# Optimization experiments

Hardware: AMD Instinct MI355X
Metric: run time of the kernel (lower is better)

Reference implementation:

```python
import jax, jax.numpy as jnp
import numpy as np

EPS = 1e-6
NEG = -100000.0


def _ln(x):
    # LayerNorm, elementwise_affine=False, eps=1e-6
    mu = jnp.mean(x, axis=-1, keepdims=True)
    var = jnp.mean((x - mu) ** 2, axis=-1, keepdims=True)
    return (x - mu) * jax.lax.rsqrt(var + EPS)


def _split_heads(x, h):
    b, s, d = x.shape
    return x.reshape(b, s, h, d // h).transpose(0, 2, 1, 3)  # [B,H,S,Dh]


def _merge_heads(x):
    b, h, s, dh = x.shape
    return x.transpose(0, 2, 1, 3).reshape(b, s, h * dh)


def _conv_pool(x, w):
    # grouped Conv2d(num_heads -> num_heads, kernel=(4,1), stride=(4,1), groups=num_heads, bias=False)
    # x: [B,H,S,Dh] as NCHW, w: [H,1,4,1] as OIHW
    return jax.lax.conv_general_dilated(
        x, w, window_strides=(4, 1), padding='VALID',
        dimension_numbers=('NCHW', 'OIHW', 'NCHW'),
        feature_group_count=x.shape[1])


def setup_inputs() -> dict:
    key = jax.random.key(0)
    ks = jax.random.split(key, 14)
    B, S, M, D, QKV, MLP, H = 4, 4096, 256, 768, 768, 3072, 12
    std = 0.02
    f = lambda k, shp: jax.random.normal(k, shp, jnp.float32) * std
    return {
        'x': jax.random.normal(ks[0], (B, S, D), jnp.float32),
        'memory': jax.random.normal(ks[1], (B, M, D), jnp.float32),
        'mask': jax.random.randint(ks[2], (B, S), 0, 2).astype(jnp.int32),
        'Wq': f(ks[3], (QKV, D)), 'Wk': f(ks[4], (QKV, D)),
        'Wv': f(ks[5], (QKV, D)), 'Wo': f(ks[6], (D, QKV)),
        'conv_w': f(ks[7], (H, 1, 4, 1)),
        'Uq': f(ks[8], (QKV, D)), 'Uk': f(ks[9], (QKV, D)),
        'Uv': f(ks[10], (QKV, D)), 'Uo': f(ks[11], (D, QKV)),
        'W1': f(ks[12], (MLP, D)), 'W2': f(ks[13], (D, MLP)),
    }


def reference(x, memory, mask, Wq, Wk, Wv, Wo, conv_w, Uq, Uk, Uv, Uo, W1, W2):
    H = conv_w.shape[0]
    maskf = mask.astype(x.dtype)                       # [B,S]

    # ---- pack: ConvAttention(memory as q, x as k/v); conv downsamples k/v ->
    #      shape_change=True so the k_mask is skipped (as in the torch code).
    q = _split_heads(memory @ Wq.T, H)                 # [B,H,M,Dh], unit temperature (log_temp=0)
    k = _split_heads(x @ Wk.T, H)                      # [B,H,S,Dh]
    v = _split_heads(x @ Wv.T, H)
    k = _conv_pool(k, conv_w)                          # [B,H,S//4,Dh]
    v = _conv_pool(v, conv_w)
    logits = jnp.einsum('bhqd,bhkd->bhqk', q, k)
    att = jax.nn.softmax(logits, axis=-1)
    packed = _merge_heads(att @ v) @ Wo.T              # [B,M,D]

    # ---- unpack: TAttention(x as q, packed as k/v) with q_mask injection
    head_dim = Uq.shape[0] // H
    uq = _split_heads(x @ Uq.T, H) * (1.0 / jnp.sqrt(jnp.asarray(head_dim, x.dtype)))
    uk = _split_heads(packed @ Uk.T, H)                # [B,H,M,Dh]
    uv = _split_heads(packed @ Uv.T, H)
    ulogits = jnp.einsum('bhqd,bhkd->bhqk', uq, uk)    # [B,H,S,M]
    ulogits = ulogits + NEG * (1.0 - maskf[:, None, :, None])
    uatt = jax.nn.softmax(ulogits, axis=-1)
    unpacked = _merge_heads(uatt @ uv) @ Uo.T          # [B,S,D]

    unpacked = unpacked * maskf[..., None]
    q_out = _ln(x + unpacked)
    m_out = _ln(memory + packed)

    # FFN: Linear -> GELU(exact) -> Linear (dropout=0)
    h = jax.nn.gelu(jnp.einsum('bsd,md->bsm', q_out, W1), approximate=False)
    y = jnp.einsum('bsm,dm->bsd', h, W2)
    y = y * maskf[..., None]
    q_out = _ln(q_out + y)
    return (q_out, m_out)
```

## Files before the change

### kernel.cpp

```cpp
#include <hip/hip_runtime.h>
#include <hip/hip_bf16.h>
#include <math.h>


typedef unsigned short u16;
typedef __attribute__((ext_vector_type(8))) short bf8v;
typedef __attribute__((ext_vector_type(4))) float f4v;
typedef __attribute__((ext_vector_type(4))) unsigned short us4v;

#define AS1 __attribute__((address_space(1)))
#define AS3 __attribute__((address_space(3)))

__device__ __forceinline__ void gld_lds16(const void* g, void* l) {
  __builtin_amdgcn_global_load_lds((const AS1 unsigned int*)g,
                                   (AS3 unsigned int*)l, 16, 0, 0);
}

__device__ __forceinline__ u16 bf16_rne(float x) {
  unsigned u = __float_as_uint(x);
  return (u16)((u + 0x7fffu + ((u >> 16) & 1u)) >> 16);
}
__device__ __forceinline__ float bf16_to_f(u16 h) {
  return __uint_as_float(((unsigned)h) << 16);
}

__global__ __launch_bounds__(256) void tobf16_kernel(
    const float* __restrict__ in, u16* __restrict__ o, int n4, float scale) {
  int i = blockIdx.x * 256 + threadIdx.x;
  if (i >= n4) return;
  float4 v = ((const float4*)in)[i];
  us4v h;
  h[0] = bf16_rne(v.x * scale); h[1] = bf16_rne(v.y * scale);
  h[2] = bf16_rne(v.z * scale); h[3] = bf16_rne(v.w * scale);
  ((us4v*)o)[i] = h;
}

template <int BN, int GELU, int OMODE>
__global__ __launch_bounds__(256) void bgemm_kernel(
    const u16* __restrict__ A, const u16* __restrict__ B,
    float* __restrict__ Cf, u16* __restrict__ Cb, int M, int N, int K,
    int lda, int ldb, int ldc, long long aSB, long long aSH, long long bSB,
    long long bSH, long long cSB, long long cSH, int HB, float scale) {
  constexpr int NJ = BN / 32;
  constexpr int LPB = BN / 64;
  __shared__ u16 smA[2][4096];
  __shared__ u16 smB[2][BN * 32];
  const int t = threadIdx.x;
  const int w = t >> 6, lane = t & 63;
  const int z = blockIdx.z;
  const int bb = z / HB, hh = z % HB;
  const u16* Ab = A + bb * aSB + hh * aSH;
  const u16* Bb = B + bb * bSB + hh * bSH;
  float* Cfb = (OMODE != 1) ? (Cf + bb * cSB + hh * cSH) : nullptr;
  u16* Cbb = (OMODE >= 1) ? (Cb + bb * cSB + hh * cSH) : nullptr;

  const int gx = gridDim.x;
  const int nwg = gx * gridDim.y;
  int f = blockIdx.x + gx * blockIdx.y;
  if ((nwg & 7) == 0) {
    const int cpx = nwg >> 3;
    f = (f & 7) * cpx + (f >> 3);
  }
  const int row0 = (f / gx) * 128, col0 = (f % gx) * BN;

  const int brow_l = lane >> 2;
  const int bchunk = ((lane & 3) ^ ((lane >> 3) & 3)) * 8;
  const int fr = lane & 15;
  const int fq = lane >> 4;
  const int fco = (fq ^ ((lane >> 1) & 3)) * 8;
  const int wr = (w >> 1) * 64, wc = (w & 1) * (BN / 2);

  f4v acc[4][NJ];
#pragma unroll
  for (int i = 0; i < 4; ++i)
#pragma unroll
    for (int j = 0; j < NJ; ++j) acc[i][j] = {0.f, 0.f, 0.f, 0.f};

  const int NT = K >> 5;

#pragma unroll
  for (int i = 0; i < 2; ++i) {
    const int g = w * 2 + i;
    const int r = g * 16 + brow_l;
    gld_lds16(Ab + (long long)(row0 + r) * lda + bchunk,
              &smA[0][g * 512 + lane * 8]);
  }
#pragma unroll
  for (int i = 0; i < LPB; ++i) {
    const int g = w * LPB + i;
    const int r = g * 16 + brow_l;
    gld_lds16(Bb + (long long)(col0 + r) * ldb + bchunk,
              &smB[0][g * 512 + lane * 8]);
  }
  __syncthreads();

  for (int tt = 0; tt < NT; ++tt) {
    const int cur = tt & 1, nxt = cur ^ 1;
    const bool more = (tt + 1) < NT;
    if (more) {
      const int k1 = (tt + 1) << 5;
#pragma unroll
      for (int i = 0; i < 2; ++i) {
        const int g = w * 2 + i;
        const int r = g * 16 + brow_l;
        gld_lds16(Ab + (long long)(row0 + r) * lda + k1 + bchunk,
                  &smA[nxt][g * 512 + lane * 8]);
      }
#pragma unroll
      for (int i = 0; i < LPB; ++i) {
        const int g = w * LPB + i;
        const int r = g * 16 + brow_l;
        gld_lds16(Bb + (long long)(col0 + r) * ldb + k1 + bchunk,
                  &smB[nxt][g * 512 + lane * 8]);
      }
    }
    {
      bf8v af[4], bfr[NJ];
#pragma unroll
      for (int mi = 0; mi < 4; ++mi)
        af[mi] = *(const bf8v*)&smA[cur][(wr + mi * 16 + fr) * 32 + fco];
#pragma unroll
      for (int nj = 0; nj < NJ; ++nj)
        bfr[nj] = *(const bf8v*)&smB[cur][(wc + nj * 16 + fr) * 32 + fco];
#pragma unroll
      for (int mi = 0; mi < 4; ++mi)
#pragma unroll
        for (int nj = 0; nj < NJ; ++nj)
          acc[mi][nj] = __builtin_amdgcn_mfma_f32_16x16x32_bf16(
              af[mi], bfr[nj], acc[mi][nj], 0, 0, 0);
    }
    __syncthreads();
  }

#pragma unroll
  for (int mi = 0; mi < 4; ++mi)
#pragma unroll
    for (int nj = 0; nj < NJ; ++nj) {
      const int col = col0 + wc + nj * 16 + fr;
      const long long base =
          (long long)(row0 + wr + mi * 16 + fq * 4) * ldc + col;
#pragma unroll
      for (int j = 0; j < 4; ++j) {
        float v = acc[mi][nj][j] * scale;
        if (GELU) v = 0.5f * v * (1.f + erff(v * 0.70710678118654752f));
        const long long idx = base + (long long)j * ldc;
        if (OMODE != 1) Cfb[idx] = v;
        if (OMODE >= 1) Cbb[idx] = bf16_rne(v);
      }
    }
}

__global__ __launch_bounds__(512) void fused_unpack_attn(
    const u16* __restrict__ q, int ldq, const u16* __restrict__ k, int ldk,
    const u16* __restrict__ vt, u16* __restrict__ o) {
  __shared__ char pool[76800];
  u16* smA = (u16*)pool;
  u16* smB = (u16*)(pool + 8192);
  u16* Pbuf = (u16*)pool;
  u16* smV = (u16*)(pool + 65536);
  float* partial = (float*)(pool + 73728);
  float* rowmax = (float*)(pool + 75776);
  float* rowsum = (float*)(pool + 76288);

  const int t = threadIdx.x;
  const int w = t >> 6, lane = t & 63;
  const int z = blockIdx.z;
  const int b = z / 12, h = z % 12;
  const int q0 = blockIdx.x * 128;

  const long long qoff = (long long)(b * 4096 + q0) * ldq + h * 64;
  const long long koff = (long long)(b * 256) * ldk + h * 64;
  const long long vbase = ((long long)(b * 12 + h)) * 16384;
  const long long ooff = (long long)(b * 4096 + q0) * 768 + h * 64;

  const int fr = lane & 15, fq = lane >> 4;
  const int fco = (fq ^ ((lane >> 1) & 3)) * 8;
  const int brow_l = lane >> 2;
  const int bchunk = ((lane & 3) ^ ((lane >> 3) & 3)) * 8;

  const int wr = (w >> 2) * 64, wc = (w & 3) * 64;
  f4v acc[4][4];
#pragma unroll
  for (int i = 0; i < 4; ++i)
#pragma unroll
    for (int j = 0; j < 4; ++j) acc[i][j] = {0.f, 0.f, 0.f, 0.f};

  for (int k0 = 0; k0 < 64; k0 += 32) {
    __syncthreads();
#pragma unroll
    for (int i = 0; i < 2; ++i) {
      const int g = w * 2 + i;
      const int r = g * 16 + brow_l;
      gld_lds16(k + koff + (long long)r * ldk + k0 + bchunk,
                smB + g * 512 + lane * 8);
    }
    {
      const int r = w * 16 + brow_l;
      gld_lds16(q + qoff + (long long)r * ldq + k0 + bchunk,
                smA + w * 512 + lane * 8);
    }
    __syncthreads();
#pragma unroll
    for (int mi = 0; mi < 4; ++mi) {
      const bf8v a0 = *(const bf8v*)&smA[(wr + mi * 16 + fr) * 32 + fco];
#pragma unroll
      for (int nj = 0; nj < 4; ++nj) {
        const bf8v b0 = *(const bf8v*)&smB[(wc + nj * 16 + fr) * 32 + fco];
        acc[mi][nj] = __builtin_amdgcn_mfma_f32_16x16x32_bf16(a0, b0, acc[mi][nj], 0, 0, 0);
      }
    }
  }
  __syncthreads();

  if (w < 4) {
    const int r = w * 16 + brow_l;
    gld_lds16(vt + vbase + (long long)r * 256 + bchunk,
              smV + w * 512 + lane * 8);
  }

#pragma unroll
  for (int mi = 0; mi < 4; ++mi)
#pragma unroll
    for (int j = 0; j < 4; ++j) {
      float m = fmaxf(fmaxf(acc[mi][0][j], acc[mi][1][j]),
                      fmaxf(acc[mi][2][j], acc[mi][3][j]));
#pragma unroll
      for (int o2 = 1; o2 < 16; o2 <<= 1) m = fmaxf(m, __shfl_xor(m, o2));
      if (fr == 0) partial[(w & 3) * 128 + wr + mi * 16 + fq * 4 + j] = m;
    }
  __syncthreads();
  if (t < 128)
    rowmax[t] = fmaxf(fmaxf(partial[t], partial[128 + t]),
                      fmaxf(partial[256 + t], partial[384 + t]));
  __syncthreads();
#pragma unroll
  for (int mi = 0; mi < 4; ++mi)
#pragma unroll
    for (int j = 0; j < 4; ++j) {
      const int row = wr + mi * 16 + fq * 4 + j;
      const float rm = rowmax[row];
      float s = 0.f;
#pragma unroll
      for (int nj = 0; nj < 4; ++nj) {
        const float e = exp2f(acc[mi][nj][j] - rm);
        s += e;
        const int col = wc + nj * 16 + fr;
        const int kc = col >> 5, kloc = col & 31;
        Pbuf[kc * 4096 + row * 32 + (((kloc >> 3) ^ ((row >> 1) & 3)) * 8) +
             (kloc & 7)] = bf16_rne(e);
      }
#pragma unroll
      for (int o2 = 1; o2 < 16; o2 <<= 1) s += __shfl_xor(s, o2);
      if (fr == 0) partial[(w & 3) * 128 + row] = s;
    }
  __syncthreads();
  if (t < 128)
    rowsum[t] = 1.f / ((partial[t] + partial[128 + t]) +
                       (partial[256 + t] + partial[384 + t]));
  __syncthreads();

  const int wrp = (w >> 1) * 32, wcp = (w & 1) * 32;
  f4v acc2[2][2];
#pragma unroll
  for (int i = 0; i < 2; ++i)
#pragma unroll
    for (int j = 0; j < 2; ++j) acc2[i][j] = {0.f, 0.f, 0.f, 0.f};

  for (int kc = 0; kc < 8; ++kc) {
    const int cur = (kc & 1) * 2048;
    if (kc < 7 && w < 4) {
      const int r = w * 16 + brow_l;
      gld_lds16(vt + vbase + (long long)r * 256 + (kc + 1) * 32 + bchunk,
                smV + (2048 - cur) + w * 512 + lane * 8);
    }
#pragma unroll
    for (int mi = 0; mi < 2; ++mi) {
      const bf8v pa =
          *(const bf8v*)&Pbuf[kc * 4096 + (wrp + mi * 16 + fr) * 32 + fco];
#pragma unroll
      for (int nj = 0; nj < 2; ++nj) {
        const bf8v v0 =
            *(const bf8v*)&smV[cur + (wcp + nj * 16 + fr) * 32 + fco];
        acc2[mi][nj] = __builtin_amdgcn_mfma_f32_16x16x32_bf16(pa, v0, acc2[mi][nj], 0, 0, 0);
      }
    }
    __syncthreads();
  }
#pragma unroll
  for (int mi = 0; mi < 2; ++mi)
#pragma unroll
    for (int nj = 0; nj < 2; ++nj)
#pragma unroll
      for (int j = 0; j < 4; ++j) {
        const int row = wrp + mi * 16 + fq * 4 + j;
        const int col = wcp + nj * 16 + fr;
        o[ooff + (long long)row * 768 + col] =
            bf16_rne(acc2[mi][nj][j] * rowsum[row]);
      }
}

__global__ __launch_bounds__(256) void conv_bf16_kernel(
    const u16* __restrict__ in, const float* __restrict__ w,
    u16* __restrict__ o, int total, int ld) {
  int idx = blockIdx.x * 256 + threadIdx.x;
  if (idx >= total) return;
  const int dh = idx & 63;
  int r = idx >> 6;
  const int tt = r & 1023; r >>= 10;
  const int h = r % 12;
  const int b = r / 12;
  const long long s = ((long long)(b * 4096 + 4 * tt)) * ld + h * 64 + dh;
  const float* wh = w + h * 4;
  float v = 0.f;
#pragma unroll
  for (int j = 0; j < 4; ++j) v = fmaf(wh[j], bf16_to_f(in[s + j * ld]), v);
  o[idx] = bf16_rne(v);
}

__global__ __launch_bounds__(256) void convT_bf16_kernel(
    const u16* __restrict__ in, const float* __restrict__ w,
    u16* __restrict__ o, int total, int ld) {
  int idx = blockIdx.x * 256 + threadIdx.x;
  if (idx >= total) return;
  const int tt = idx & 1023;
  int r = idx >> 10;
  const int dh = r & 63; r >>= 6;
  const int h = r % 12;
  const int b = r / 12;
  const long long s = ((long long)(b * 4096 + 4 * tt)) * ld + h * 64 + dh;
  const float* wh = w + h * 4;
  float v = 0.f;
#pragma unroll
  for (int j = 0; j < 4; ++j) v = fmaf(wh[j], bf16_to_f(in[s + j * ld]), v);
  o[idx] = bf16_rne(v);
}

__global__ __launch_bounds__(256) void transT_b2b_kernel(
    const u16* __restrict__ in, u16* __restrict__ o, int total, int ld) {
  int idx = blockIdx.x * 256 + threadIdx.x;
  if (idx >= total) return;
  const int key = idx & 255;
  int r = idx >> 8;
  const int dh = r & 63; r >>= 6;
  const int h = r % 12;
  const int b = r / 12;
  o[idx] = in[((long long)(b * 256 + key)) * ld + h * 64 + dh];
}

__global__ __launch_bounds__(256) void softmax_ip_kernel(float* __restrict__ data) {
  const long long row = blockIdx.x;
  float* p = data + row * 1024;
  u16* ob = (u16*)p;
  const int t = threadIdx.x;
  __shared__ float red[4];
  float v[4];
  float lmax = -3.4e38f;
#pragma unroll
  for (int i = 0; i < 4; ++i) {
    v[i] = p[t + (i << 8)];
    lmax = fmaxf(lmax, v[i]);
  }
  for (int o = 32; o; o >>= 1) lmax = fmaxf(lmax, __shfl_xor(lmax, o));
  if ((t & 63) == 0) red[t >> 6] = lmax;
  __syncthreads();
  const float gmax = fmaxf(fmaxf(red[0], red[1]), fmaxf(red[2], red[3]));
  float lsum = 0.f;
#pragma unroll
  for (int i = 0; i < 4; ++i) {
    v[i] = expf(v[i] - gmax);
    lsum += v[i];
  }
  __syncthreads();
  for (int o = 32; o; o >>= 1) lsum += __shfl_xor(lsum, o);
  if ((t & 63) == 0) red[t >> 6] = lsum;
  __syncthreads();
  const float inv = 1.f / (red[0] + red[1] + red[2] + red[3]);
#pragma unroll
  for (int i = 0; i < 4; ++i) ob[t + (i << 8)] = bf16_rne(v[i] * inv);
}

__global__ __launch_bounds__(256) void ln_kernel(
    const float* __restrict__ a, const float* __restrict__ b,
    const int* __restrict__ mask, float* __restrict__ out,
    u16* __restrict__ outb) {
  const long long row = blockIdx.x;
  const float* pa = a + row * 768;
  const float* pb = b + row * 768;
  const float ms = mask ? (float)mask[row] : 1.f;
  __shared__ float buf[768];
  __shared__ float red[4];
  const int t = threadIdx.x;
  float lsum = 0.f;
#pragma unroll
  for (int i = t; i < 768; i += 256) {
    const float v = fmaf(pb[i], ms, pa[i]);
    buf[i] = v;
    lsum += v;
  }
  for (int o = 32; o; o >>= 1) lsum += __shfl_xor(lsum, o);
  if ((t & 63) == 0) red[t >> 6] = lsum;
  __syncthreads();
  const float mu = (red[0] + red[1] + red[2] + red[3]) * (1.f / 768.f);
  float lvar = 0.f;
#pragma unroll
  for (int i = t; i < 768; i += 256) {
    const float d = buf[i] - mu;
    lvar = fmaf(d, d, lvar);
  }
  __syncthreads();
  for (int o = 32; o; o >>= 1) lvar += __shfl_xor(lvar, o);
  if ((t & 63) == 0) red[t >> 6] = lvar;
  __syncthreads();
  const float var = (red[0] + red[1] + red[2] + red[3]) * (1.f / 768.f);
  const float rstd = rsqrtf(var + 1e-6f);
  float* po = out + row * 768;
  u16* pob = outb ? outb + row * 768 : nullptr;
#pragma unroll
  for (int i = t; i < 768; i += 256) {
    const float v = (buf[i] - mu) * rstd;
    po[i] = v;
    if (outb) pob[i] = bf16_rne(v);
  }
}

static inline void tobf16(hipStream_t st, const float* in, u16* o, int n,
                          float scale = 1.f) {
  int n4 = n / 4;
  tobf16_kernel<<<(n4 + 255) / 256, 256, 0, st>>>(in, o, n4, scale);
}

extern "C" void kernel_launch(void* const* d_in, const int* in_sizes, int n_in,
                              void* d_out, int out_size, void* d_ws,
                              size_t ws_size, hipStream_t stream) {
  const float* x = (const float*)d_in[0];
  const float* memory = (const float*)d_in[1];
  const int* mask = (const int*)d_in[2];
  const float* Wq = (const float*)d_in[3];
  const float* Wk = (const float*)d_in[4];
  const float* Wv = (const float*)d_in[5];
  const float* Wo = (const float*)d_in[6];
  const float* conv_w = (const float*)d_in[7];
  const float* Uq = (const float*)d_in[8];
  const float* Uk = (const float*)d_in[9];
  const float* Uv = (const float*)d_in[10];
  const float* Uo = (const float*)d_in[11];
  const float* W1 = (const float*)d_in[12];
  const float* W2 = (const float*)d_in[13];
  float* out = (float*)d_out;
  float* ws = (float*)d_ws;

  const int XR = 16384, MR = 1024, D = 768, MLP = 3072;
  const long long CB = 3145728;
  const int WD = 589824;
  const int WM = 2359296;

  float* A0 = ws + 0;
  float* A1 = ws + 18874368;
  float* A2 = ws + 31457280;

  u16* xb    = (u16*)(A0 + 12582912);
  u16* kvqb  = (u16*)A0;
  float* logits = A1;
  u16* attb  = (u16*)A1;
  u16* uattvb = (u16*)A1;
  float* unp = A0;
  u16* qout1b = (u16*)(out + 6291456);
  u16* hb    = (u16*)A1;
  float* ybuf = A2;

  u16* kpb  = (u16*)A2;
  u16* vpTb = kpb + 3145728;
  u16* qpb  = (u16*)(A2 + 3145728);
  u16* memb = qpb + 786432;
  u16* avmb = (u16*)(A2 + 3932160);
  u16* pkb  = avmb + 786432;
  float* packed = A2 + 4718592;
  u16* ukvb = (u16*)(A2 + 5505024);
  u16* uvTb = (u16*)(A2 + 6291456);
  u16* wp16 = (u16*)(A2 + 7077888);

  u16* Wkvqb = wp16;
  u16* Wqb = wp16 + 2304 * 768;
  u16* Wob = Wqb + WD;
  u16* Ukvb2 = wp16;
  u16* Uob = wp16 + 1536 * 768;
  u16* W1b = wp16;
  u16* W2b = wp16 + WM;

  tobf16(stream, x, xb, 12582912);
  tobf16(stream, memory, memb, 786432);
  tobf16(stream, Wk, Wkvqb, WD);
  tobf16(stream, Wv, Wkvqb + WD, WD);
  tobf16(stream, Uq, Wkvqb + 2 * WD, WD, 0.18033688011112042592f);
  tobf16(stream, Wq, Wqb, WD);
  tobf16(stream, Wo, Wob, WD);
  bgemm_kernel<128, 0, 1><<<dim3(18, 128, 1), 256, 0, stream>>>(
      xb, Wkvqb, nullptr, kvqb, XR, 2304, D, D, D, 2304,
      0, 0, 0, 0, 0, 0, 1, 1.f);
  bgemm_kernel<128, 0, 1><<<dim3(6, 8, 1), 256, 0, stream>>>(
      memb, Wqb, nullptr, qpb, MR, D, D, D, D, D, 0, 0, 0, 0, 0, 0, 1, 1.f);
  conv_bf16_kernel<<<12288, 256, 0, stream>>>(kvqb, conv_w, kpb, 3145728, 2304);
  convT_bf16_kernel<<<12288, 256, 0, stream>>>(kvqb + 768, conv_w, vpTb, 3145728, 2304);
  bgemm_kernel<128, 0, 0><<<dim3(8, 2, 48), 256, 0, stream>>>(
      qpb, kpb, logits, nullptr, 256, 1024, 64, 768, 64, 1024,
      196608, 64, 786432, 65536, 3145728, 262144, 12, 1.f);
  softmax_ip_kernel<<<12288, 256, 0, stream>>>(logits);
  bgemm_kernel<64, 0, 1><<<dim3(1, 2, 48), 256, 0, stream>>>(
      attb, vpTb, nullptr, avmb, 256, 64, 1024, 2048, 1024, 768,
      6291456, 524288, 786432, 65536, 196608, 64, 12, 1.f);
  bgemm_kernel<128, 0, 2><<<dim3(6, 8, 1), 256, 0, stream>>>(
      avmb, Wob, packed, pkb, MR, D, D, D, D, D, 0, 0, 0, 0, 0, 0, 1, 1.f);
  ln_kernel<<<MR, 256, 0, stream>>>(memory, packed, nullptr, out + 12582912,
                                    nullptr);

  tobf16(stream, Uk, Ukvb2, WD);
  tobf16(stream, Uv, Ukvb2 + WD, WD);
  tobf16(stream, Uo, Uob, WD);
  bgemm_kernel<128, 0, 1><<<dim3(12, 8, 1), 256, 0, stream>>>(
      pkb, Ukvb2, nullptr, ukvb, MR, 1536, D, D, D, 1536,
      0, 0, 0, 0, 0, 0, 1, 1.f);
  transT_b2b_kernel<<<3072, 256, 0, stream>>>(ukvb + 768, uvTb, 786432, 1536);
  {
    dim3 g(32, 1, 48);
    fused_unpack_attn<<<g, 512, 0, stream>>>(kvqb + 1536, 2304, ukvb, 1536,
                                             uvTb, uattvb);
  }
  bgemm_kernel<128, 0, 0><<<dim3(6, 32, 4), 256, 0, stream>>>(
      uattvb, Uob, unp, nullptr, 4096, D, D, D, D, D,
      CB, 0, 0, 0, CB, 0, 1, 1.f);
  ln_kernel<<<XR, 256, 0, stream>>>(x, unp, mask, unp, qout1b);

  tobf16(stream, W1, W1b, WM);
  tobf16(stream, W2, W2b, WM);
  for (int c = 0; c < 2; ++c) {
    bgemm_kernel<128, 1, 1><<<dim3(24, 32, 2), 256, 0, stream>>>(
        qout1b + (long long)c * 2 * CB, W1b, nullptr, hb, 4096, MLP, D,
        D, D, MLP, CB, 0, 0, 0, 12582912, 0, 1, 1.f);
    bgemm_kernel<128, 0, 0><<<dim3(6, 32, 2), 256, 0, stream>>>(
        hb, W2b, ybuf, nullptr, 4096, D, MLP, MLP, MLP, D,
        12582912, 0, 0, 0, CB, 0, 1, 1.f);
    ln_kernel<<<8192, 256, 0, stream>>>(unp + (long long)c * 2 * CB, ybuf,
                                        mask + c * 8192,
                                        out + (long long)c * 2 * CB, nullptr);
  }
}
```

Baseline: 700.7 us.

## Fuse pack attention into flash-style kernel and batch bf16 conversions

Replaces the pack-attention sequence (logits GEMM writing fp32 to global, in-place softmax, then the P·V GEMM) with a single online-softmax kernel. It keeps Q and P in LDS and uses exp2 with log2(e) folded into the query projection scale. It also merges the many small fp32-to-bf16 weight and input conversion launches into multi-segment kernels to cut launch overhead. The fused kernel uses only 96 blocks with about 110KB of LDS each, so occupancy is low and the GPU may be underused.

After: 684.2 us. 1.02x faster.

```diff
diff --git a/kernel.cpp b/kernel.cpp
--- a/kernel.cpp
+++ b/kernel.cpp
@@ -24,15 +24,26 @@
   return __uint_as_float(((unsigned)h) << 16);
 }
 
-__global__ __launch_bounds__(256) void tobf16_kernel(
-    const float* __restrict__ in, u16* __restrict__ o, int n4, float scale) {
-  int i = blockIdx.x * 256 + threadIdx.x;
-  if (i >= n4) return;
-  float4 v = ((const float4*)in)[i];
+struct Cvt8 {
+  const float* src[8];
+  u16* dst[8];
+  int n4[8];
+  float sc[8];
+  int cum[9];
+  int ns;
+};
+__global__ __launch_bounds__(256) void tobf16_multi_kernel(Cvt8 c) {
+  int b = blockIdx.x;
+  int seg = 0;
+  while (seg + 1 < c.ns && b >= c.cum[seg + 1]) ++seg;
+  int i = (b - c.cum[seg]) * 256 + threadIdx.x;
+  if (i >= c.n4[seg]) return;
+  const float sc = c.sc[seg];
+  float4 v = ((const float4*)c.src[seg])[i];
   us4v h;
-  h[0] = bf16_rne(v.x * scale); h[1] = bf16_rne(v.y * scale);
-  h[2] = bf16_rne(v.z * scale); h[3] = bf16_rne(v.w * scale);
-  ((us4v*)o)[i] = h;
+  h[0] = bf16_rne(v.x * sc); h[1] = bf16_rne(v.y * sc);
+  h[2] = bf16_rne(v.z * sc); h[3] = bf16_rne(v.w * sc);
+  ((us4v*)c.dst[seg])[i] = h;
 }
 
 template <int BN, int GELU, int OMODE>
@@ -150,6 +161,185 @@
     }
 }
 
+__global__ __launch_bounds__(512) void fused_pack_attn(
+    const u16* __restrict__ q, const u16* __restrict__ k,
+    const u16* __restrict__ vt, u16* __restrict__ o) {
+  __shared__ char pool[110080];
+  u16* smQ = (u16*)pool;
+  u16* smK = (u16*)(pool + 16384);
+  u16* Pbuf = (u16*)(pool + 32768);
+  u16* smV = (u16*)(pool + 98304);
+  float* partial = (float*)(pool + 106496);
+  float* mold = (float*)(pool + 108544);
+  float* fbuf = (float*)(pool + 109056);
+  float* srow = (float*)(pool + 109568);
+
+  const int t = threadIdx.x;
+  const int w = t >> 6, lane = t & 63;
+  const int z = blockIdx.z;
+  const int b = z / 12, h = z % 12;
+  const int qrow0 = b * 256 + blockIdx.x * 128;
+  const long long kvbase = ((long long)(b * 12 + h)) * 65536;
+
+  const int fr = lane & 15, fq = lane >> 4;
+  const int fco = (fq ^ ((lane >> 1) & 3)) * 8;
+  const int brow_l = lane >> 2;
+  const int bchunk = ((lane & 3) ^ ((lane >> 3) & 3)) * 8;
+  const int wr = (w >> 2) * 64, wc = (w & 3) * 64;
+  const int wrp = (w >> 1) * 32, wcp = (w & 1) * 32;
+
+#pragma unroll
+  for (int i = 0; i < 2; ++i) {
+    const int g = w * 2 + i;
+    const int plane = g >> 3, grp = g & 7;
+    gld_lds16(q + (long long)(qrow0 + grp * 16 + brow_l) * 768 + h * 64 +
+                  plane * 32 + bchunk,
+              smQ + plane * 4096 + grp * 512 + lane * 8);
+  }
+  if (t < 128) {
+    mold[t] = -3.0e38f;
+    srow[t] = 0.f;
+  }
+
+  f4v acc2[2][2];
+#pragma unroll
+  for (int i = 0; i < 2; ++i)
+#pragma unroll
+    for (int j = 0; j < 2; ++j) acc2[i][j] = {0.f, 0.f, 0.f, 0.f};
+
+  for (int kc = 0; kc < 4; ++kc) {
+    f4v acc[4][4];
+#pragma unroll
+    for (int i = 0; i < 4; ++i)
+#pragma unroll
+      for (int j = 0; j < 4; ++j) acc[i][j] = {0.f, 0.f, 0.f, 0.f};
+
+#pragma unroll
+    for (int khalf = 0; khalf < 2; ++khalf) {
+      __syncthreads();
+#pragma unroll
+      for (int i = 0; i < 2; ++i) {
+        const int g = w * 2 + i;
+        gld_lds16(k + kvbase +
+                      (long long)(kc * 256 + g * 16 + brow_l) * 64 +
+                      khalf * 32 + bchunk,
+                  smK + g * 512 + lane * 8);
+      }
+      __syncthreads();
+#pragma unroll
+      for (int mi = 0; mi < 4; ++mi) {
+        const bf8v a0 =
+            *(const bf8v*)&smQ[khalf * 4096 + (wr + mi * 16 + fr) * 32 + fco];
+#pragma unroll
+        for (int nj = 0; nj < 4; ++nj) {
+          const bf8v b0 = *(const bf8v*)&smK[(wc + nj * 16 + fr) * 32 + fco];
+          acc[mi][nj] =
+              __builtin_amdgcn_mfma_f32_16x16x32_bf16(a0, b0, acc[mi][nj], 0, 0, 0);
+        }
+      }
+    }
+    __syncthreads();
+
+#pragma unroll
+    for (int mi = 0; mi < 4; ++mi)
+#pragma unroll
+      for (int j = 0; j < 4; ++j) {
+        float m = fmaxf(fmaxf(acc[mi][0][j], acc[mi][1][j]),
+                        fmaxf(acc[mi][2][j], acc[mi][3][j]));
+#pragma unroll
+        for (int o2 = 1; o2 < 16; o2 <<= 1) m = fmaxf(m, __shfl_xor(m, o2));
+        if (fr == 0) partial[(w & 3) * 128 + wr + mi * 16 + fq * 4 + j] = m;
+      }
+    __syncthreads();
+    if (t < 128) {
+      const float cm = fmaxf(fmaxf(partial[t], partial[128 + t]),
+                             fmaxf(partial[256 + t], partial[384 + t]));
+      const float mnew = fmaxf(mold[t], cm);
+      fbuf[t] = exp2f(mold[t] - mnew);
+      mold[t] = mnew;
+    }
+    __syncthreads();
+
+#pragma unroll
+    for (int mi = 0; mi < 4; ++mi)
+#pragma unroll
+      for (int j = 0; j < 4; ++j) {
+        const int row = wr + mi * 16 + fq * 4 + j;
+        const float rm = mold[row];
+        float s = 0.f;
+#pragma unroll
+        for (int nj = 0; nj < 4; ++nj) {
+          const float e = exp2f(acc[mi][nj][j] - rm);
+          s += e;
+          const int col = wc + nj * 16 + fr;
+          const int kc2 = col >> 5, kloc = col & 31;
+          Pbuf[kc2 * 4096 + row * 32 + (((kloc >> 3) ^ ((row >> 1) & 3)) * 8) +
+               (kloc & 7)] = bf16_rne(e);
+        }
+#pragma unroll
+        for (int o2 = 1; o2 < 16; o2 <<= 1) s += __shfl_xor(s, o2);
+        if (fr == 0) partial[(w & 3) * 128 + row] = s;
+      }
+    if (w < 4) {
+      gld_lds16(vt + kvbase + (long long)(w * 16 + brow_l) * 1024 + kc * 256 +
+                    bchunk,
+                smV + w * 512 + lane * 8);
+    }
+    __syncthreads();
+    if (t < 128)
+      srow[t] = srow[t] * fbuf[t] +
+                ((partial[t] + partial[128 + t]) +
+                 (partial[256 + t] + partial[384 + t]));
+    __syncthreads();
+
+#pragma unroll
+    for (int mi = 0; mi < 2; ++mi)
+#pragma unroll
+      for (int j = 0; j < 4; ++j) {
+        const float fr_ = fbuf[wrp + mi * 16 + fq * 4 + j];
+        acc2[mi][0][j] *= fr_;
+        acc2[mi][1][j] *= fr_;
+      }
+
+    for (int sk = 0; sk < 8; ++sk) {
+      const int cur = (sk & 1) * 2048;
+      if (sk < 7 && w < 4) {
+        gld_lds16(vt + kvbase + (long long)(w * 16 + brow_l) * 1024 +
+                      kc * 256 + (sk + 1) * 32 + bchunk,
+                  smV + (2048 - cur) + w * 512 + lane * 8);
+      }
+#pragma unroll
+      for (int mi = 0; mi < 2; ++mi) {
+        const bf8v pa =
+            *(const bf8v*)&Pbuf[sk * 4096 + (wrp + mi * 16 + fr) * 32 + fco];
+#pragma unroll
+        for (int nj = 0; nj < 2; ++nj) {
+          const bf8v v0 =
+              *(const bf8v*)&smV[cur + (wcp + nj * 16 + fr) * 32 + fco];
+          acc2[mi][nj] =
+              __builtin_amdgcn_mfma_f32_16x16x32_bf16(pa, v0, acc2[mi][nj], 0, 0, 0);
+        }
+      }
+      __syncthreads();
+    }
+  }
+
+  if (t < 128) fbuf[t] = 1.f / srow[t];
+  __syncthreads();
+  const long long ooff = (long long)qrow0 * 768 + h * 64;
+#pragma unroll
+  for (int mi = 0; mi < 2; ++mi)
+#pragma unroll
+    for (int nj = 0; nj < 2; ++nj)
+#pragma unroll
+      for (int j = 0; j < 4; ++j) {
+        const int row = wrp + mi * 16 + fq * 4 + j;
+        const int col = wcp + nj * 16 + fr;
+        o[ooff + (long long)row * 768 + col] =
+            bf16_rne(acc2[mi][nj][j] * fbuf[row]);
+      }
+}
+
 __global__ __launch_bounds__(512) void fused_unpack_attn(
     const u16* __restrict__ q, int ldq, const u16* __restrict__ k, int ldk,
     const u16* __restrict__ vt, u16* __restrict__ o) {
@@ -347,38 +537,6 @@
   o[idx] = in[((long long)(b * 256 + key)) * ld + h * 64 + dh];
 }
 
-__global__ __launch_bounds__(256) void softmax_ip_kernel(float* __restrict__ data) {
-  const long long row = blockIdx.x;
-  float* p = data + row * 1024;
-  u16* ob = (u16*)p;
-  const int t = threadIdx.x;
-  __shared__ float red[4];
-  float v[4];
-  float lmax = -3.4e38f;
-#pragma unroll
-  for (int i = 0; i < 4; ++i) {
-    v[i] = p[t + (i << 8)];
-    lmax = fmaxf(lmax, v[i]);
-  }
-  for (int o = 32; o; o >>= 1) lmax = fmaxf(lmax, __shfl_xor(lmax, o));
-  if ((t & 63) == 0) red[t >> 6] = lmax;
-  __syncthreads();
-  const float gmax = fmaxf(fmaxf(red[0], red[1]), fmaxf(red[2], red[3]));
-  float lsum = 0.f;
-#pragma unroll
-  for (int i = 0; i < 4; ++i) {
-    v[i] = expf(v[i] - gmax);
-    lsum += v[i];
-  }
-  __syncthreads();
-  for (int o = 32; o; o >>= 1) lsum += __shfl_xor(lsum, o);
-  if ((t & 63) == 0) red[t >> 6] = lsum;
-  __syncthreads();
-  const float inv = 1.f / (red[0] + red[1] + red[2] + red[3]);
-#pragma unroll
-  for (int i = 0; i < 4; ++i) ob[t + (i << 8)] = bf16_rne(v[i] * inv);
-}
-
 __global__ __launch_bounds__(256) void ln_kernel(
     const float* __restrict__ a, const float* __restrict__ b,
     const int* __restrict__ mask, float* __restrict__ out,
@@ -421,12 +579,6 @@
     po[i] = v;
     if (outb) pob[i] = bf16_rne(v);
   }
-}
-
-static inline void tobf16(hipStream_t st, const float* in, u16* o, int n,
-                          float scale = 1.f) {
-  int n4 = n / 4;
-  tobf16_kernel<<<(n4 + 255) / 256, 256, 0, st>>>(in, o, n4, scale);
 }
 
 extern "C" void kernel_launch(void* const* d_in, const int* in_sizes, int n_in,
@@ -460,8 +612,6 @@
 
   u16* xb    = (u16*)(A0 + 12582912);
   u16* kvqb  = (u16*)A0;
-  float* logits = A1;
-  u16* attb  = (u16*)A1;
   u16* uattvb = (u16*)A1;
   float* unp = A0;
   u16* qout1b = (u16*)(out + 6291456);
@@ -487,35 +637,51 @@
   u16* W1b = wp16;
   u16* W2b = wp16 + WM;
 
-  tobf16(stream, x, xb, 12582912);
-  tobf16(stream, memory, memb, 786432);
-  tobf16(stream, Wk, Wkvqb, WD);
-  tobf16(stream, Wv, Wkvqb + WD, WD);
-  tobf16(stream, Uq, Wkvqb + 2 * WD, WD, 0.18033688011112042592f);
-  tobf16(stream, Wq, Wqb, WD);
-  tobf16(stream, Wo, Wob, WD);
+  const float UQS = 0.18033688011112042592f;
+  const float L2E = 1.4426950408889634074f;
+
+  {
+    Cvt8 c{};
+    const float* ss[7] = {x, memory, Wk, Wv, Uq, Wq, Wo};
+    u16* dd[7] = {xb, memb, Wkvqb, Wkvqb + WD, Wkvqb + 2 * WD, Wqb, Wob};
+    int nn[7] = {3145728, 196608, WD / 4, WD / 4, WD / 4, WD / 4, WD / 4};
+    float sc[7] = {1.f, 1.f, 1.f, 1.f, UQS, 1.f, 1.f};
+    int cum = 0;
+    for (int i = 0; i < 7; ++i) {
+      c.src[i] = ss[i]; c.dst[i] = dd[i]; c.n4[i] = nn[i]; c.sc[i] = sc[i];
+      c.cum[i] = cum; cum += (nn[i] + 255) / 256;
+    }
+    c.cum[7] = cum; c.ns = 7;
+    tobf16_multi_kernel<<<cum, 256, 0, stream>>>(c);
+  }
   bgemm_kernel<128, 0, 1><<<dim3(18, 128, 1), 256, 0, stream>>>(
       xb, Wkvqb, nullptr, kvqb, XR, 2304, D, D, D, 2304,
       0, 0, 0, 0, 0, 0, 1, 1.f);
   bgemm_kernel<128, 0, 1><<<dim3(6, 8, 1), 256, 0, stream>>>(
-      memb, Wqb, nullptr, qpb, MR, D, D, D, D, D, 0, 0, 0, 0, 0, 0, 1, 1.f);
+      memb, Wqb, nullptr, qpb, MR, D, D, D, D, D, 0, 0, 0, 0, 0, 0, 1, L2E);
   conv_bf16_kernel<<<12288, 256, 0, stream>>>(kvqb, conv_w, kpb, 3145728, 2304);
   convT_bf16_kernel<<<12288, 256, 0, stream>>>(kvqb + 768, conv_w, vpTb, 3145728, 2304);
-  bgemm_kernel<128, 0, 0><<<dim3(8, 2, 48), 256, 0, stream>>>(
-      qpb, kpb, logits, nullptr, 256, 1024, 64, 768, 64, 1024,
-      196608, 64, 786432, 65536, 3145728, 262144, 12, 1.f);
-  softmax_ip_kernel<<<12288, 256, 0, stream>>>(logits);
-  bgemm_kernel<64, 0, 1><<<dim3(1, 2, 48), 256, 0, stream>>>(
-      attb, vpTb, nullptr, avmb, 256, 64, 1024, 2048, 1024, 768,
-      6291456, 524288, 786432, 65536, 196608, 64, 12, 1.f);
+  {
+    dim3 g(2, 1, 48);
+    fused_pack_attn<<<g, 512, 0, stream>>>(qpb, kpb, vpTb, avmb);
+  }
   bgemm_kernel<128, 0, 2><<<dim3(6, 8, 1), 256, 0, stream>>>(
       avmb, Wob, packed, pkb, MR, D, D, D, D, D, 0, 0, 0, 0, 0, 0, 1, 1.f);
   ln_kernel<<<MR, 256, 0, stream>>>(memory, packed, nullptr, out + 12582912,
                                     nullptr);
 
-  tobf16(stream, Uk, Ukvb2, WD);
-  tobf16(stream, Uv, Ukvb2 + WD, WD);
-  tobf16(stream, Uo, Uob, WD);
+  {
+    Cvt8 c{};
+    const float* ss[3] = {Uk, Uv, Uo};
+    u16* dd[3] = {Ukvb2, Ukvb2 + WD, Uob};
+    int cum = 0;
+    for (int i = 0; i < 3; ++i) {
+      c.src[i] = ss[i]; c.dst[i] = dd[i]; c.n4[i] = WD / 4; c.sc[i] = 1.f;
+      c.cum[i] = cum; cum += (WD / 4 + 255) / 256;
+    }
+    c.cum[3] = cum; c.ns = 3;
+    tobf16_multi_kernel<<<cum, 256, 0, stream>>>(c);
+  }
   bgemm_kernel<128, 0, 1><<<dim3(12, 8, 1), 256, 0, stream>>>(
       pkb, Ukvb2, nullptr, ukvb, MR, 1536, D, D, D, 1536,
       0, 0, 0, 0, 0, 0, 1, 1.f);
@@ -530,8 +696,18 @@
       CB, 0, 0, 0, CB, 0, 1, 1.f);
   ln_kernel<<<XR, 256, 0, stream>>>(x, unp, mask, unp, qout1b);
 
-  tobf16(stream, W1, W1b, WM);
-  tobf16(stream, W2, W2b, WM);
+  {
+    Cvt8 c{};
+    const float* ss[2] = {W1, W2};
+    u16* dd[2] = {W1b, W2b};
+    int cum = 0;
+    for (int i = 0; i < 2; ++i) {
+      c.src[i] = ss[i]; c.dst[i] = dd[i]; c.n4[i] = WM / 4; c.sc[i] = 1.f;
+      c.cum[i] = cum; cum += (WM / 4 + 255) / 256;
+    }
+    c.cum[2] = cum; c.ns = 2;
+    tobf16_multi_kernel<<<cum, 256, 0, stream>>>(c);
+  }
   for (int c = 0; c < 2; ++c) {
     bgemm_kernel<128, 1, 1><<<dim3(24, 32, 2), 256, 0, stream>>>(
         qout1b + (long long)c * 2 * CB, W1b, nullptr, hb, 4096, MLP, D,
```
